# Optimization experiments

Measured on AMD Instinct MI355X. Metric: run time of the kernel, lower is better.

The kernel has to match this reference:

```python
import jax, jax.numpy as jnp
import numpy as np

D_MODEL = 512
D_EMB = 300
D_FIXED = 30000
D_EXT = 32000
BS, L, J, N, T = 8, 256, 48, 32, 48


def setup_inputs() -> dict:
    key = jax.random.key(0)
    ks = jax.random.split(key, 32)
    s = 0.02
    def nrm(k, shape, scale=0.02):
        return jax.random.normal(k, shape, dtype=jnp.float32) * scale
    inp = {
        "Mp": jax.random.normal(ks[0], (BS, L, D_MODEL), dtype=jnp.float32),
        "Mq": jax.random.normal(ks[1], (BS, J, D_MODEL), dtype=jnp.float32),
        "Mqa": jax.random.normal(ks[2], (BS, N, D_MODEL), dtype=jnp.float32),
        "Mnlg": jax.random.normal(ks[3], (BS, T, D_MODEL), dtype=jnp.float32),
        "mask_p": jnp.ones((BS, L, 1), dtype=bool),
        "mask_q": jnp.ones((BS, J, 1), dtype=bool),
        "mask_qa": jnp.ones((BS, N, 1), dtype=bool),
        "source_ext": jax.random.randint(ks[4], (BS, L + J + N), 0, D_EXT, dtype=jnp.int64) if jax.config.jax_enable_x64 else jax.random.randint(ks[4], (BS, L + J + N), 0, D_EXT).astype(jnp.int32),
        "special_mask": jnp.ones((D_FIXED,), dtype=bool).at[jnp.array([0, 1, 2, 3])].set(False),
        "d_ext_vocab": D_EXT,
    }
    # additive attention params for question / qa / passage branches
    names = ["q", "a", "p"]
    for i, nme in enumerate(names):
        base = 5 + 5 * i
        inp[f"Wk_{nme}"] = nrm(ks[base + 0], (D_MODEL, D_MODEL))
        inp[f"bk_{nme}"] = jnp.zeros((D_MODEL,), dtype=jnp.float32)
        inp[f"Wq_{nme}"] = nrm(ks[base + 1], (D_MODEL, D_MODEL))
        inp[f"bq_{nme}"] = jnp.zeros((D_MODEL,), dtype=jnp.float32)
        inp[f"v_{nme}"] = nrm(ks[base + 2], (D_MODEL,))
    # vocab generator: Linear(d_model, d_emb) -> Linear(d_emb, d_fixed, bias=False)
    inp["W1"] = nrm(ks[20], (D_MODEL, D_EMB))
    inp["b1"] = jnp.zeros((D_EMB,), dtype=jnp.float32)
    inp["W2"] = nrm(ks[21], (D_EMB, D_FIXED))
    # mixture: Linear(4*d_model, 4) + softmax
    inp["Wm"] = nrm(ks[22], (4 * D_MODEL, 4))
    inp["bm"] = jnp.zeros((4,), dtype=jnp.float32)
    return inp


def _additive_attn(K, V, Q, mask, Wk, bk, Wq, bq, v):
    # K,V: [b,S,d]; Q: [b,T,d]; mask: [b,S,1] bool
    Kp = K @ Wk + bk                                  # [b,S,d]
    Qp = Q @ Wq + bq                                  # [b,T,d]
    scores = jnp.einsum("btsd,d->bts", jnp.tanh(Qp[:, :, None, :] + Kp[:, None, :, :]), v)
    scores = jnp.where(mask[:, None, :, 0], scores, -1e9)
    attn = jax.nn.softmax(scores, axis=-1)            # [b,T,S]
    ctx = jnp.einsum("bts,bsd->btd", attn, V)         # [b,T,d]
    return ctx, attn


def reference(Mp, Mq, Mqa, Mnlg, mask_p, mask_q, mask_qa, source_ext, special_mask,
              Wk_q, bk_q, Wq_q, bq_q, v_q,
              Wk_a, bk_a, Wq_a, bq_a, v_a,
              Wk_p, bk_p, Wq_p, bq_p, v_p,
              W1, b1, W2, Wm, bm, d_ext_vocab):
    d_fixed = special_mask.shape[0]
    bs, Tq, _ = Mnlg.shape

    ctx_q, q_distr = _additive_attn(Mq, Mq, Mnlg, mask_q, Wk_q, bk_q, Wq_q, bq_q, v_q)
    ctx_a, qa_distr = _additive_attn(Mqa, Mqa, Mnlg, mask_qa, Wk_a, bk_a, Wq_a, bq_a, v_a)
    ctx_p, p_distr = _additive_attn(Mp, Mp, Mnlg, mask_p, Wk_p, bk_p, Wq_p, bq_p, v_p)

    # fixed-vocab distribution with special tokens masked out
    logits = (Mnlg @ W1 + b1) @ W2                    # [b,T,d_fixed]
    logits = jnp.where(special_mask[None, None, :], logits, -1e9)
    fixed_vocab_distr = jax.nn.softmax(logits, axis=-1)

    # mixture weights
    mix_in = jnp.concatenate([Mnlg, ctx_q, ctx_a, ctx_p], axis=-1)  # [b,T,4d]
    lambdas = jax.nn.softmax(mix_in @ Wm + bm, axis=-1)             # [b,T,4]
    lam_v, lam_q, lam_qa, lam_p = jnp.split(lambdas, 4, axis=-1)

    fixed_vocab_distr = fixed_vocab_distr * lam_v
    source_distr = jnp.concatenate([p_distr * lam_p, q_distr * lam_q, qa_distr * lam_qa], axis=-1)  # [b,T,S_tot]

    # scatter-add over extended vocab (math-equivalent to one_hot + matmul)
    def _scatter(src, idx):
        # src: [T,S_tot], idx: [S_tot]
        return jnp.zeros((Tq, d_ext_vocab), src.dtype).at[:, idx].add(src)

    ext_vocab_distr = jax.vmap(_scatter)(source_distr, source_ext)  # [b,T,d_ext]
    ext_vocab_distr = ext_vocab_distr.at[:, :, :d_fixed].add(fixed_vocab_distr)
    return ext_vocab_distr, lambdas
```

## Files before the change

### kernel.cpp

```cpp
#include <hip/hip_runtime.h>
#include <math.h>

#define BS     8
#define LL     256
#define JJ     48
#define NN     32
#define TT     48
#define DM     512
#define DEMB   300
#define DFIX   30000
#define DEXT   32000
#define SRC_TOT (LL + JJ + NN)
#define ROWS   (BS * TT)
#define NT     235

typedef float f32x4  __attribute__((ext_vector_type(4)));
typedef short bf16x8 __attribute__((ext_vector_type(8)));

__device__ __forceinline__ short f2bf(float f) {
    union { float f; unsigned u; } v; v.f = f;
    return (short)((v.u + 0x7FFFu + ((v.u >> 16) & 1u)) >> 16);
}
__device__ __forceinline__ float bf2f(short s) {
    union { unsigned u; float f; } v;
    v.u = ((unsigned)(unsigned short)s) << 16;
    return v.f;
}
__device__ __forceinline__ float fast_exp2(float x) {
#if __has_builtin(__builtin_amdgcn_exp2f)
    return __builtin_amdgcn_exp2f(x);
#else
    return exp2f(x);
#endif
}
__device__ __forceinline__ float fast_rcp(float x) {
#if __has_builtin(__builtin_amdgcn_rcpf)
    return __builtin_amdgcn_rcpf(x);
#else
    return 1.f / x;
#endif
}
__device__ __forceinline__ float fast_tanh(float x) {
    x = fminf(fmaxf(x, -15.f), 15.f);
    const float e = fast_exp2(x * 2.885390082f);
    return (e - 1.f) * fast_rcp(e + 1.f);
}
__device__ __forceinline__ bool smask_true(const void* smask, bool byteLayout, int i)
{
    if (byteLayout) return ((const unsigned char*)smask)[i] != 0;
    return ((const int*)smask)[i] != 0;
}
__device__ __forceinline__ void mask8(const void* smask, bool byteLayout, int i,
                                      int* mb)
{
    if (byteLayout) {
        const uchar4 a = ((const uchar4*)((const unsigned char*)smask + i))[0];
        const uchar4 b = ((const uchar4*)((const unsigned char*)smask + i))[1];
        mb[0]=a.x; mb[1]=a.y; mb[2]=a.z; mb[3]=a.w;
        mb[4]=b.x; mb[5]=b.y; mb[6]=b.z; mb[7]=b.w;
    } else {
        const int* p = (const int*)smask + i;
        #pragma unroll
        for (int j = 0; j < 8; ++j) mb[j] = p[j];
    }
}

struct PDesc { const float* src; short* dst; int K, N, Kp, ntx, tiles; };
struct PArgs { PDesc d[8]; int nd; };

__global__ __launch_bounds__(256) void prep_kernel(PArgs pa)
{
    __shared__ short T[64][72];
    int tile = blockIdx.x, g = 0;
    while (g + 1 < pa.nd && tile >= pa.d[g].tiles) { tile -= pa.d[g].tiles; ++g; }
    const PDesc d = pa.d[g];
    const int kt = tile / d.ntx, nt = tile % d.ntx;
    const int k0 = kt * 64, n0 = nt * 64;
    const int tid = threadIdx.x;
    {
        const int n = n0 + (tid & 63);
        #pragma unroll
        for (int p = 0; p < 16; ++p) {
            const int kk = p * 4 + (tid >> 6);
            const int k = k0 + kk;
            float v = 0.f;
            if (k < d.K && n < d.N) v = d.src[(size_t)k * d.N + n];
            T[kk][tid & 63] = f2bf(v);
        }
    }
    __syncthreads();
    {
        const int nn = tid >> 2;
        const int kq = (tid & 3) * 16;
        const int n = n0 + nn;
        if (n < d.N) {
            bf16x8 v0, v1;
            #pragma unroll
            for (int j = 0; j < 8; ++j) v0[j] = T[kq + j][nn];
            #pragma unroll
            for (int j = 0; j < 8; ++j) v1[j] = T[kq + 8 + j][nn];
            *(bf16x8*)&d.dst[(size_t)n * d.Kp + k0 + kq]     = v0;
            *(bf16x8*)&d.dst[(size_t)n * d.Kp + k0 + kq + 8] = v1;
        }
    }
}

struct GDesc { const float* A; const short* Bt; const float* bias; void* C;
               const void* smask; float* pstat;
               int M, N, K, Kp, nx, my, obf, nt, tiles; };
struct GArgs { GDesc d[7]; int nd; };

__global__ __launch_bounds__(256) void gemm_bf16_kernel(GArgs ga)
{
    __shared__ short As[2][4][130][8];
    __shared__ short Bs[2][4][130][8];
    __shared__ float pm_s[128][2];
    __shared__ float ps_s[128][2];

    int tile = blockIdx.x, g = 0;
    while (g + 1 < ga.nd && tile >= ga.d[g].tiles) { tile -= ga.d[g].tiles; ++g; }
    const float* __restrict__ A  = ga.d[g].A;
    const short* __restrict__ Bt = ga.d[g].Bt;
    const float* bias = ga.d[g].bias;
    const int N = ga.d[g].N, K = ga.d[g].K, Kp = ga.d[g].Kp;
    const int nx = ga.d[g].nx, my = ga.d[g].my, obf = ga.d[g].obf;

    int bm, bn;
    if (my > 0) { bm = (tile % my) * 128; bn = (tile / my) * 128; }
    else        { bm = (tile / nx) * 128; bn = (tile % nx) * 128; }
    const int tid  = threadIdx.x;
    const int lane = tid & 63;
    const int wv   = tid >> 6;
    const int wm   = (wv >> 1) * 64;
    const int wn   = (wv & 1) * 64;

    const int a_kq  = (tid & 7) * 4;
    const int a_row = tid >> 3;
    float4  ra[4];
    bf16x8  rb[2];

    auto loadA = [&](int k0) {
        #pragma unroll
        for (int p = 0; p < 4; ++p) {
            const int row = p * 32 + a_row;
            const int gk = k0 + a_kq;
            const float* ap = A + (size_t)(bm + row) * K + gk;
            float4 a = make_float4(0.f, 0.f, 0.f, 0.f);
            if (gk + 3 < K) a = *(const float4*)ap;
            else {
                if (gk     < K) a.x = ap[0];
                if (gk + 1 < K) a.y = ap[1];
                if (gk + 2 < K) a.z = ap[2];
                if (gk + 3 < K) a.w = ap[3];
            }
            ra[p] = a;
        }
    };
    auto loadB = [&](int k0) {
        #pragma unroll
        for (int p = 0; p < 2; ++p) {
            const int idx = p * 256 + tid;
            const int n = idx >> 2, kb = idx & 3;
            const int gn = bn + n;
            bf16x8 v = {};
            if (gn < N) v = *(const bf16x8*)&Bt[(size_t)gn * Kp + k0 + kb * 8];
            rb[p] = v;
        }
    };
    auto storeA = [&](int buf) {
        const int kb = a_kq >> 3, ko = a_kq & 7;
        #pragma unroll
        for (int p = 0; p < 4; ++p) {
            const int row = p * 32 + a_row;
            short4 s = { f2bf(ra[p].x), f2bf(ra[p].y), f2bf(ra[p].z), f2bf(ra[p].w) };
            *(short4*)&As[buf][kb][row][ko] = s;
        }
    };
    auto storeB = [&](int buf) {
        #pragma unroll
        for (int p = 0; p < 2; ++p) {
            const int idx = p * 256 + tid;
            const int n = idx >> 2, kb = idx & 3;
            *(bf16x8*)&Bs[buf][kb][n][0] = rb[p];
        }
    };

    f32x4 acc[4][4] = {};
    const int nk = Kp / 32;

    loadA(0); loadB(0);
    storeA(0); storeB(0);
    __syncthreads();

    for (int kk = 0; kk < nk; ++kk) {
        const int cur = kk & 1;
        if (kk + 1 < nk) { loadA((kk + 1) * 32); loadB((kk + 1) * 32); }
        bf16x8 af[4], bfr[4];
        #pragma unroll
        for (int i = 0; i < 4; ++i) {
            af[i]  = *(const bf16x8*)&As[cur][lane >> 4][wm + i * 16 + (lane & 15)][0];
            bfr[i] = *(const bf16x8*)&Bs[cur][lane >> 4][wn + i * 16 + (lane & 15)][0];
        }
        #pragma unroll
        for (int mi = 0; mi < 4; ++mi)
            #pragma unroll
            for (int ni = 0; ni < 4; ++ni)
                acc[mi][ni] = __builtin_amdgcn_mfma_f32_16x16x32_bf16(
                    af[mi], bfr[ni], acc[mi][ni], 0, 0, 0);
        if (kk + 1 < nk) { storeA(cur ^ 1); storeB(cur ^ 1); }
        __syncthreads();
    }

    if (!obf) {
        float* Cf = (float*)ga.d[g].C;
        #pragma unroll
        for (int ni = 0; ni < 4; ++ni) {
            const int gn = bn + wn + ni * 16 + (lane & 15);
            if (gn >= N) continue;
            const float bb = bias ? bias[gn] : 0.f;
            #pragma unroll
            for (int mi = 0; mi < 4; ++mi)
                #pragma unroll
                for (int r = 0; r < 4; ++r) {
                    const int gm = bm + wm + mi * 16 + (lane >> 4) * 4 + r;
                    Cf[(size_t)gm * N + gn] = acc[mi][ni][r] + bb;
                }
        }
    } else {
        short* Cs = (short*)ga.d[g].C;
        const void* sm = ga.d[g].smask;
        const bool byteLayout = (((const int*)sm)[1] == 0x01010101);
        int mk[4];
        #pragma unroll
        for (int ni = 0; ni < 4; ++ni) {
            const int gn = bn + wn + ni * 16 + (lane & 15);
            const bool inb = (gn < N);
            mk[ni] = inb && smask_true(sm, byteLayout, inb ? gn : 0);
            if (inb) {
                #pragma unroll
                for (int mi = 0; mi < 4; ++mi)
                    #pragma unroll
                    for (int r = 0; r < 4; ++r) {
                        const int gm = bm + wm + mi * 16 + (lane >> 4) * 4 + r;
                        Cs[(size_t)gm * N + gn] = f2bf(acc[mi][ni][r]);
                    }
            }
        }
        #pragma unroll
        for (int mi = 0; mi < 4; ++mi) {
            #pragma unroll
            for (int r = 0; r < 4; ++r) {
                const int rl = wm + mi * 16 + (lane >> 4) * 4 + r;
                float vmax = -INFINITY;
                #pragma unroll
                for (int ni = 0; ni < 4; ++ni)
                    if (mk[ni]) vmax = fmaxf(vmax, acc[mi][ni][r]);
                #pragma unroll
                for (int o = 1; o < 16; o <<= 1)
                    vmax = fmaxf(vmax, __shfl_xor(vmax, o));
                float se = 0.f;
                #pragma unroll
                for (int ni = 0; ni < 4; ++ni)
                    if (mk[ni]) se += __expf(acc[mi][ni][r] - vmax);
                #pragma unroll
                for (int o = 1; o < 16; o <<= 1)
                    se += __shfl_xor(se, o);
                if ((lane & 15) == 0) {
                    pm_s[rl][wn >> 6] = vmax;
                    ps_s[rl][wn >> 6] = se;
                }
            }
        }
        __syncthreads();
        if (tid < 128) {
            const float mA = pm_s[tid][0], mB = pm_s[tid][1];
            const float sA = ps_s[tid][0], sB = ps_s[tid][1];
            const float m = fmaxf(mA, mB);
            float s = 0.f;
            if (sA > 0.f) s += sA * __expf(mA - m);
            if (sB > 0.f) s += sB * __expf(mB - m);
            float* ps = ga.d[g].pstat;
            const size_t idx = ((size_t)(bm + tid) * ga.d[g].nt + (bn >> 7)) * 2;
            ps[idx + 0] = m;
            ps[idx + 1] = s;
        }
    }
}

__global__ __launch_bounds__(64) void combine_kernel(
    const float* __restrict__ pstat, const float* __restrict__ lam,
    float* __restrict__ stat)
{
    const int r = blockIdx.x;
    const int lane = threadIdx.x;
    float m = -INFINITY;
    for (int c = lane; c < NT; c += 64)
        m = fmaxf(m, pstat[((size_t)r * NT + c) * 2]);
    #pragma unroll
    for (int o = 32; o; o >>= 1) m = fmaxf(m, __shfl_xor(m, o));
    float s = 0.f;
    for (int c = lane; c < NT; c += 64) {
        const float pm = pstat[((size_t)r * NT + c) * 2];
        const float ps = pstat[((size_t)r * NT + c) * 2 + 1];
        if (ps > 0.f) s += ps * __expf(pm - m);
    }
    #pragma unroll
    for (int o = 32; o; o >>= 1) s += __shfl_xor(s, o);
    if (lane == 0) {
        stat[r * 2 + 0] = m;
        stat[r * 2 + 1] = lam[r * 4 + 0] / s;
    }
}

struct SDesc { const float* Kp; const float* Qp; const float* vv;
               int Sb, s0, cnt, off; };
struct SArgs { SDesc c[6]; };

__global__ __launch_bounds__(256) void scores_kernel(SArgs sa,
                                                     float* __restrict__ scb)
{
    const SDesc d = sa.c[blockIdx.y];
    const int bt   = blockIdx.x;
    const int b    = bt / TT;
    const int tid  = threadIdx.x;
    const int lane = tid & 63;
    const int wave = tid >> 6;

    float qp[8], vv[8];
    {
        const float4* q4 = (const float4*)(d.Qp + (size_t)bt * DM) + lane * 2;
        float4 a = q4[0], c = q4[1];
        qp[0]=a.x; qp[1]=a.y; qp[2]=a.z; qp[3]=a.w;
        qp[4]=c.x; qp[5]=c.y; qp[6]=c.z; qp[7]=c.w;
        const float4* v4 = (const float4*)d.vv + lane * 2;
        a = v4[0]; c = v4[1];
        vv[0]=a.x; vv[1]=a.y; vv[2]=a.z; vv[3]=a.w;
        vv[4]=c.x; vv[5]=c.y; vv[6]=c.z; vv[7]=c.w;
    }
    for (int s = wave; s < d.cnt; s += 4) {
        const float* krow = d.Kp + ((size_t)b * d.Sb + d.s0 + s) * DM + lane * 8;
        const float4 ka = ((const float4*)krow)[0];
        const float4 kb = ((const float4*)krow)[1];
        float acc = 0.f;
        acc = fmaf(vv[0], fast_tanh(qp[0] + ka.x), acc);
        acc = fmaf(vv[1], fast_tanh(qp[1] + ka.y), acc);
        acc = fmaf(vv[2], fast_tanh(qp[2] + ka.z), acc);
        acc = fmaf(vv[3], fast_tanh(qp[3] + ka.w), acc);
        acc = fmaf(vv[4], fast_tanh(qp[4] + kb.x), acc);
        acc = fmaf(vv[5], fast_tanh(qp[5] + kb.y), acc);
        acc = fmaf(vv[6], fast_tanh(qp[6] + kb.z), acc);
        acc = fmaf(vv[7], fast_tanh(qp[7] + kb.w), acc);
        #pragma unroll
        for (int off = 32; off; off >>= 1) acc += __shfl_xor(acc, off);
        if (lane == 0) scb[(size_t)bt * SRC_TOT + d.off + s] = acc;
    }
}

__global__ __launch_bounds__(512) void attn2mix_kernel(
    const float* __restrict__ scb,
    const float* __restrict__ Mq, const float* __restrict__ Mqa,
    const float* __restrict__ Mp, const float* __restrict__ Mnlg,
    const float* __restrict__ Wm, const float* __restrict__ bm,
    float* __restrict__ dQ, float* __restrict__ dQA, float* __restrict__ dP,
    float* __restrict__ lam_ws, float* __restrict__ lam_out)
{
    __shared__ float a_sh[SRC_TOT];
    __shared__ float cQ[DM], cA[DM], cP[DM];
    __shared__ float red[16];
    __shared__ float redm[32];
    const int bt   = blockIdx.x;
    const int b    = bt / TT;
    const int tid  = threadIdx.x;
    const int lane = tid & 63;
    const int wave = tid >> 6;
    const float* srow = scb + (size_t)bt * SRC_TOT;

    #pragma unroll
    for (int br = 0; br < 3; ++br) {
        const int off = (br == 0) ? 0 : (br == 1) ? JJ : (JJ + NN);
        const int cnt = (br == 0) ? JJ : (br == 1) ? NN : LL;
        float x = (tid < cnt) ? srow[off + tid] : -INFINITY;
        float m = x;
        #pragma unroll
        for (int o = 32; o; o >>= 1) m = fmaxf(m, __shfl_xor(m, o));
        if (lane == 0) red[wave] = m;
        __syncthreads();
        m = red[0];
        #pragma unroll
        for (int w = 1; w < 8; ++w) m = fmaxf(m, red[w]);
        float e = (tid < cnt) ? __expf(x - m) : 0.f;
        float ss = e;
        #pragma unroll
        for (int o = 32; o; o >>= 1) ss += __shfl_xor(ss, o);
        if (lane == 0) red[8 + wave] = ss;
        __syncthreads();
        float denom = 0.f;
        #pragma unroll
        for (int w = 0; w < 8; ++w) denom += red[8 + w];
        if (tid < cnt) {
            const float a = e / denom;
            a_sh[off + tid] = a;
            float* dst = (br == 0) ? dQ : (br == 1) ? dQA : dP;
            dst[(size_t)bt * cnt + tid] = a;
        }
        __syncthreads();
    }
    {
        float aQ = 0.f, aA = 0.f, aP = 0.f;
        for (int s = 0; s < JJ; ++s)
            aQ = fmaf(a_sh[s],           Mq [((size_t)b * JJ + s) * DM + tid], aQ);
        for (int s = 0; s < NN; ++s)
            aA = fmaf(a_sh[JJ + s],      Mqa[((size_t)b * NN + s) * DM + tid], aA);
        for (int s = 0; s < LL; ++s)
            aP = fmaf(a_sh[JJ + NN + s], Mp [((size_t)b * LL + s) * DM + tid], aP);
        cQ[tid] = aQ; cA[tid] = aA; cP[tid] = aP;
    }
    __syncthreads();
    {
        const float x0 = Mnlg[(size_t)bt * DM + tid];
        const float x1 = cQ[tid], x2 = cA[tid], x3 = cP[tid];
        const float4 w0 = *(const float4*)&Wm[(size_t)tid * 4];
        const float4 w1 = *(const float4*)&Wm[(size_t)(512 + tid) * 4];
        const float4 w2 = *(const float4*)&Wm[(size_t)(1024 + tid) * 4];
        const float4 w3 = *(const float4*)&Wm[(size_t)(1536 + tid) * 4];
        float acc[4];
        acc[0] = x0 * w0.x + x1 * w1.x + x2 * w2.x + x3 * w3.x;
        acc[1] = x0 * w0.y + x1 * w1.y + x2 * w2.y + x3 * w3.y;
        acc[2] = x0 * w0.z + x1 * w1.z + x2 * w2.z + x3 * w3.z;
        acc[3] = x0 * w0.w + x1 * w1.w + x2 * w2.w + x3 * w3.w;
        #pragma unroll
        for (int c = 0; c < 4; ++c)
            #pragma unroll
            for (int o = 32; o; o >>= 1) acc[c] += __shfl_xor(acc[c], o);
        if (lane == 0) {
            redm[wave * 4 + 0] = acc[0]; redm[wave * 4 + 1] = acc[1];
            redm[wave * 4 + 2] = acc[2]; redm[wave * 4 + 3] = acc[3];
        }
        __syncthreads();
        if (tid == 0) {
            float l[4];
            #pragma unroll
            for (int c = 0; c < 4; ++c) {
                float s = bm[c];
                #pragma unroll
                for (int w = 0; w < 8; ++w) s += redm[w * 4 + c];
                l[c] = s;
            }
            const float mx = fmaxf(fmaxf(l[0], l[1]), fmaxf(l[2], l[3]));
            const float e0 = __expf(l[0] - mx), e1 = __expf(l[1] - mx);
            const float e2 = __expf(l[2] - mx), e3 = __expf(l[3] - mx);
            const float inv = 1.f / (e0 + e1 + e2 + e3);
            lam_ws[bt * 4 + 0] = e0 * inv; lam_out[bt * 4 + 0] = e0 * inv;
            lam_ws[bt * 4 + 1] = e1 * inv; lam_out[bt * 4 + 1] = e1 * inv;
            lam_ws[bt * 4 + 2] = e2 * inv; lam_out[bt * 4 + 2] = e2 * inv;
            lam_ws[bt * 4 + 3] = e3 * inv; lam_out[bt * 4 + 3] = e3 * inv;
        }
    }
}

__global__ __launch_bounds__(1024) void writescatter_kernel(
    const short* __restrict__ logits, const void* __restrict__ smask,
    const float* __restrict__ stat, const float* __restrict__ lam,
    const float* __restrict__ dP, const float* __restrict__ dQ,
    const float* __restrict__ dQA, const void* __restrict__ src_ext,
    float* __restrict__ out)
{
    const bool byteLayout = (((const int*)smask)[1] == 0x01010101);
    const int r = blockIdx.x;
    const float m   = stat[r * 2 + 0];
    const float inv = stat[r * 2 + 1];

    const short* lrow = logits + (size_t)r * DFIX;
    float* orow = out + (size_t)r * DEXT;
    const int tid = threadIdx.x;
    #pragma unroll
    for (int k = 0; k < 4; ++k) {
        const int i = (k * 1024 + tid) * 8;
        if (i >= DEXT) continue;
        float4 o0 = make_float4(0.f, 0.f, 0.f, 0.f);
        float4 o1 = make_float4(0.f, 0.f, 0.f, 0.f);
        if (i < DFIX) {
            const bf16x8 v = *(const bf16x8*)&lrow[i];
            int mb[8]; mask8(smask, byteLayout, i, mb);
            o0.x = mb[0] ? __expf(bf2f(v[0]) - m) * inv : 0.f;
            o0.y = mb[1] ? __expf(bf2f(v[1]) - m) * inv : 0.f;
            o0.z = mb[2] ? __expf(bf2f(v[2]) - m) * inv : 0.f;
            o0.w = mb[3] ? __expf(bf2f(v[3]) - m) * inv : 0.f;
            o1.x = mb[4] ? __expf(bf2f(v[4]) - m) * inv : 0.f;
            o1.y = mb[5] ? __expf(bf2f(v[5]) - m) * inv : 0.f;
            o1.z = mb[6] ? __expf(bf2f(v[6]) - m) * inv : 0.f;
            o1.w = mb[7] ? __expf(bf2f(v[7]) - m) * inv : 0.f;
        }
        *(float4*)&orow[i]     = o0;
        *(float4*)&orow[i + 4] = o1;
    }
    __syncthreads();
    if (tid < SRC_TOT) {
        const int* s32 = (const int*)src_ext;
        const bool src64 = (s32[1] == 0 && s32[3] == 0 && s32[5] == 0 && s32[7] == 0);
        const int b = r / TT;
        const float lamq  = lam[r * 4 + 1];
        const float lamqa = lam[r * 4 + 2];
        const float lamp  = lam[r * 4 + 3];
        const int pos = b * SRC_TOT + tid;
        const int idx = src64 ? (int)((const long long*)src_ext)[pos] : s32[pos];
        float val;
        if      (tid < LL)      val = dP [(size_t)r * LL + tid]             * lamp;
        else if (tid < LL + JJ) val = dQ [(size_t)r * JJ + (tid - LL)]      * lamq;
        else                    val = dQA[(size_t)r * NN + (tid - LL - JJ)] * lamqa;
        atomicAdd(&orow[idx], val);
    }
}

extern "C" void kernel_launch(void* const* d_in, const int* in_sizes, int n_in,
                              void* d_out, int out_size, void* d_ws, size_t ws_size,
                              hipStream_t stream)
{
    const float* Mp   = (const float*)d_in[0];
    const float* Mq   = (const float*)d_in[1];
    const float* Mqa  = (const float*)d_in[2];
    const float* Mnlg = (const float*)d_in[3];
    const void* src_ext = d_in[7];
    const void* smask   = d_in[8];
    const float* Wk_q = (const float*)d_in[10];
    const float* bk_q = (const float*)d_in[11];
    const float* Wq_q = (const float*)d_in[12];
    const float* bq_q = (const float*)d_in[13];
    const float* v_q  = (const float*)d_in[14];
    const float* Wk_a = (const float*)d_in[15];
    const float* bk_a = (const float*)d_in[16];
    const float* Wq_a = (const float*)d_in[17];
    const float* bq_a = (const float*)d_in[18];
    const float* v_a  = (const float*)d_in[19];
    const float* Wk_p = (const float*)d_in[20];
    const float* bk_p = (const float*)d_in[21];
    const float* Wq_p = (const float*)d_in[22];
    const float* bq_p = (const float*)d_in[23];
    const float* v_p  = (const float*)d_in[24];
    const float* W1   = (const float*)d_in[25];
    const float* b1   = (const float*)d_in[26];
    const float* W2   = (const float*)d_in[27];
    const float* Wm   = (const float*)d_in[28];
    const float* bm   = (const float*)d_in[29];
    float* out = (float*)d_out;

    char* ws = (char*)d_ws;
    size_t off = 0;
    auto alloc = [&](size_t bytes) -> char* {
        char* p = ws + off;
        off += (bytes + 255) & ~(size_t)255;
        return p;
    };
    short* logits = (short*)alloc((size_t)ROWS * DFIX * 2);
    float* KpP    = (float*)alloc((size_t)BS * LL * DM * 4);
    float* KpQ    = (float*)alloc((size_t)BS * JJ * DM * 4);
    float* KpA    = (float*)alloc((size_t)BS * NN * DM * 4);
    float* QpQ    = (float*)alloc((size_t)ROWS * DM * 4);
    float* QpA    = (float*)alloc((size_t)ROWS * DM * 4);
    float* QpP    = (float*)alloc((size_t)ROWS * DM * 4);
    float* Hh     = (float*)alloc((size_t)ROWS * DEMB * 4);
    float* dP     = (float*)alloc((size_t)ROWS * LL * 4);
    float* dQ     = (float*)alloc((size_t)ROWS * JJ * 4);
    float* dQA    = (float*)alloc((size_t)ROWS * NN * 4);
    float* lam    = (float*)alloc((size_t)ROWS * 4 * 4);
    float* pstat  = (float*)alloc((size_t)ROWS * NT * 2 * 4);
    float* stat   = (float*)alloc((size_t)ROWS * 2 * 4);
    float* scb    = (float*)alloc((size_t)ROWS * SRC_TOT * 4);
    short* tWkq = (short*)alloc((size_t)DM * DM * 2);
    short* tWqq = (short*)alloc((size_t)DM * DM * 2);
    short* tWka = (short*)alloc((size_t)DM * DM * 2);
    short* tWqa = (short*)alloc((size_t)DM * DM * 2);
    short* tWkp = (short*)alloc((size_t)DM * DM * 2);
    short* tWqp = (short*)alloc((size_t)DM * DM * 2);
    short* tW1  = (short*)alloc((size_t)DEMB * DM * 2);
    short* tW2  = (short*)alloc((size_t)DFIX * 320 * 2);
    (void)ws_size; (void)in_sizes; (void)n_in; (void)out_size;

    PArgs pa;
    pa.nd = 8;
    pa.d[0] = { Wk_p, tWkp, DM,   DM,   DM,  8,  64 };
    pa.d[1] = { Wk_q, tWkq, DM,   DM,   DM,  8,  64 };
    pa.d[2] = { Wk_a, tWka, DM,   DM,   DM,  8,  64 };
    pa.d[3] = { Wq_q, tWqq, DM,   DM,   DM,  8,  64 };
    pa.d[4] = { Wq_a, tWqa, DM,   DM,   DM,  8,  64 };
    pa.d[5] = { Wq_p, tWqp, DM,   DM,   DM,  8,  64 };
    pa.d[6] = { W1,   tW1,  DM,   DEMB, DM,  5,  40 };
    pa.d[7] = { W2,   tW2,  DEMB, DFIX, 320, 469, 2345 };
    prep_kernel<<<64 * 6 + 40 + 2345, 256, 0, stream>>>(pa);

    GArgs gA;
    gA.nd = 1;
    gA.d[0] = { Mnlg, tW1, b1, Hh, nullptr, nullptr,
                ROWS, DEMB, DM, DM, 3, 0, 0, 0, 9 };
    gemm_bf16_kernel<<<9, 256, 0, stream>>>(gA);

    GArgs gB;
    gB.nd = 7;
    gB.d[0] = { Mp,   tWkp, bk_p,    KpP,    nullptr, nullptr,
                BS*LL, DM,   DM,   DM,  4,   0, 0, 0,  64 };
    gB.d[1] = { Mq,   tWkq, bk_q,    KpQ,    nullptr, nullptr,
                BS*JJ, DM,   DM,   DM,  4,   0, 0, 0,  12 };
    gB.d[2] = { Mqa,  tWka, bk_a,    KpA,    nullptr, nullptr,
                BS*NN, DM,   DM,   DM,  4,   0, 0, 0,   8 };
    gB.d[3] = { Mnlg, tWqq, bq_q,    QpQ,    nullptr, nullptr,
                ROWS,  DM,   DM,   DM,  4,   0, 0, 0,  12 };
    gB.d[4] = { Mnlg, tWqa, bq_a,    QpA,    nullptr, nullptr,
                ROWS,  DM,   DM,   DM,  4,   0, 0, 0,  12 };
    gB.d[5] = { Mnlg, tWqp, bq_p,    QpP,    nullptr, nullptr,
                ROWS,  DM,   DM,   DM,  4,   0, 0, 0,  12 };
    gB.d[6] = { Hh,   tW2,  nullptr, logits, smask,   pstat,
                ROWS,  DFIX, DEMB, 320, 235, 3, 1, NT, 705 };
    gemm_bf16_kernel<<<825, 256, 0, stream>>>(gB);

    SArgs sa;
    sa.c[0] = { KpQ, QpQ, v_q, JJ,   0, JJ,  0 };
    sa.c[1] = { KpA, QpA, v_a, NN,   0, NN,  JJ };
    sa.c[2] = { KpP, QpP, v_p, LL,   0, 64,  JJ + NN };
    sa.c[3] = { KpP, QpP, v_p, LL,  64, 64,  JJ + NN + 64 };
    sa.c[4] = { KpP, QpP, v_p, LL, 128, 64,  JJ + NN + 128 };
    sa.c[5] = { KpP, QpP, v_p, LL, 192, 64,  JJ + NN + 192 };
    scores_kernel<<<dim3(ROWS, 6), 256, 0, stream>>>(sa, scb);
    attn2mix_kernel<<<ROWS, 512, 0, stream>>>(scb, Mq, Mqa, Mp, Mnlg, Wm, bm,
                                              dQ, dQA, dP, lam,
                                              out + (size_t)ROWS * DEXT);

    combine_kernel<<<ROWS, 64, 0, stream>>>(pstat, lam, stat);
    writescatter_kernel<<<ROWS, 1024, 0, stream>>>(
        logits, smask, stat, lam, dP, dQ, dQA, src_ext, out);
}
```

Baseline: 161.9 us.

## Pre-convert activations to bf16 in prep kernel and fuse combine into attn2mix

Adds flat fp32-to-bf16 conversion tiles to the prep kernel for Mp, Mq, Mqa and Mnlg. The GEMMs now load bf16 A operands directly, and the first GEMM writes its hidden output as padded bf16, which removes per-tile conversion and halves A-side traffic. The attention-context reduction now reads the bf16 copies, and the separate combine kernel is folded into attn2mix, saving one launch. In exchange the prep kernel does extra conversion work, and the context vectors now use bf16 inputs, which lowers their precision.

```diff
diff --git a/kernel.cpp b/kernel.cpp
--- a/kernel.cpp
+++ b/kernel.cpp
@@ -13,6 +13,7 @@
 #define SRC_TOT (LL + JJ + NN)
 #define ROWS   (BS * TT)
 #define NT     235
+#define KH     320
 
 typedef float f32x4  __attribute__((ext_vector_type(4)));
 typedef short bf16x8 __attribute__((ext_vector_type(8)));
@@ -66,7 +67,7 @@
 }
 
 struct PDesc { const float* src; short* dst; int K, N, Kp, ntx, tiles; };
-struct PArgs { PDesc d[8]; int nd; };
+struct PArgs { PDesc d[12]; int nd; };
 
 __global__ __launch_bounds__(256) void prep_kernel(PArgs pa)
 {
@@ -74,9 +75,23 @@
     int tile = blockIdx.x, g = 0;
     while (g + 1 < pa.nd && tile >= pa.d[g].tiles) { tile -= pa.d[g].tiles; ++g; }
     const PDesc d = pa.d[g];
+    const int tid = threadIdx.x;
+
+    if (d.ntx == 0) {
+        const int i = (tile * 256 + tid) * 8;
+        if (i < d.K) {
+            const float4 a = ((const float4*)(d.src + i))[0];
+            const float4 b = ((const float4*)(d.src + i))[1];
+            bf16x8 v;
+            v[0]=f2bf(a.x); v[1]=f2bf(a.y); v[2]=f2bf(a.z); v[3]=f2bf(a.w);
+            v[4]=f2bf(b.x); v[5]=f2bf(b.y); v[6]=f2bf(b.z); v[7]=f2bf(b.w);
+            *(bf16x8*)&d.dst[i] = v;
+        }
+        return;
+    }
+
     const int kt = tile / d.ntx, nt = tile % d.ntx;
     const int k0 = kt * 64, n0 = nt * 64;
-    const int tid = threadIdx.x;
     {
         const int n = n0 + (tid & 63);
         #pragma unroll
@@ -105,9 +120,9 @@
     }
 }
 
-struct GDesc { const float* A; const short* Bt; const float* bias; void* C;
+struct GDesc { const short* A; const short* Bt; const float* bias; void* C;
                const void* smask; float* pstat;
-               int M, N, K, Kp, nx, my, obf, nt, tiles; };
+               int M, N, K, Kp, nx, my, obf, npad, nt, tiles; };
 struct GArgs { GDesc d[7]; int nd; };
 
 __global__ __launch_bounds__(256) void gemm_bf16_kernel(GArgs ga)
@@ -119,11 +134,12 @@
 
     int tile = blockIdx.x, g = 0;
     while (g + 1 < ga.nd && tile >= ga.d[g].tiles) { tile -= ga.d[g].tiles; ++g; }
-    const float* __restrict__ A  = ga.d[g].A;
+    const short* __restrict__ A  = ga.d[g].A;
     const short* __restrict__ Bt = ga.d[g].Bt;
     const float* bias = ga.d[g].bias;
-    const int N = ga.d[g].N, K = ga.d[g].K, Kp = ga.d[g].Kp;
+    const int N = ga.d[g].N, Kp = ga.d[g].Kp;
     const int nx = ga.d[g].nx, my = ga.d[g].my, obf = ga.d[g].obf;
+    const int npad = ga.d[g].npad;
 
     int bm, bn;
     if (my > 0) { bm = (tile % my) * 128; bn = (tile / my) * 128; }
@@ -134,26 +150,13 @@
     const int wm   = (wv >> 1) * 64;
     const int wn   = (wv & 1) * 64;
 
-    const int a_kq  = (tid & 7) * 4;
-    const int a_row = tid >> 3;
-    float4  ra[4];
-    bf16x8  rb[2];
+    bf16x8 ra[2], rb[2];
 
     auto loadA = [&](int k0) {
         #pragma unroll
-        for (int p = 0; p < 4; ++p) {
-            const int row = p * 32 + a_row;
-            const int gk = k0 + a_kq;
-            const float* ap = A + (size_t)(bm + row) * K + gk;
-            float4 a = make_float4(0.f, 0.f, 0.f, 0.f);
-            if (gk + 3 < K) a = *(const float4*)ap;
-            else {
-                if (gk     < K) a.x = ap[0];
-                if (gk + 1 < K) a.y = ap[1];
-                if (gk + 2 < K) a.z = ap[2];
-                if (gk + 3 < K) a.w = ap[3];
-            }
-            ra[p] = a;
+        for (int p = 0; p < 2; ++p) {
+            const int row = p * 64 + (tid >> 2);
+            ra[p] = *(const bf16x8*)&A[(size_t)(bm + row) * Kp + k0 + (tid & 3) * 8];
         }
     };
     auto loadB = [&](int k0) {
@@ -168,13 +171,10 @@
         }
     };
     auto storeA = [&](int buf) {
-        const int kb = a_kq >> 3, ko = a_kq & 7;
-        #pragma unroll
-        for (int p = 0; p < 4; ++p) {
-            const int row = p * 32 + a_row;
-            short4 s = { f2bf(ra[p].x), f2bf(ra[p].y), f2bf(ra[p].z), f2bf(ra[p].w) };
-            *(short4*)&As[buf][kb][row][ko] = s;
-        }
+        const int kb = tid & 3;
+        #pragma unroll
+        for (int p = 0; p < 2; ++p)
+            *(bf16x8*)&As[buf][kb][p * 64 + (tid >> 2)][0] = ra[p];
     };
     auto storeB = [&](int buf) {
         #pragma unroll
@@ -211,7 +211,7 @@
         __syncthreads();
     }
 
-    if (!obf) {
+    if (obf == 0) {
         float* Cf = (float*)ga.d[g].C;
         #pragma unroll
         for (int ni = 0; ni < 4; ++ni) {
@@ -224,6 +224,22 @@
                 for (int r = 0; r < 4; ++r) {
                     const int gm = bm + wm + mi * 16 + (lane >> 4) * 4 + r;
                     Cf[(size_t)gm * N + gn] = acc[mi][ni][r] + bb;
+                }
+        }
+    } else if (obf == 2) {
+        short* Cs = (short*)ga.d[g].C;
+        #pragma unroll
+        for (int ni = 0; ni < 4; ++ni) {
+            const int gn = bn + wn + ni * 16 + (lane & 15);
+            if (gn >= npad) continue;
+            const bool valid = (gn < N);
+            const float bb = (valid && bias) ? bias[gn] : 0.f;
+            #pragma unroll
+            for (int mi = 0; mi < 4; ++mi)
+                #pragma unroll
+                for (int r = 0; r < 4; ++r) {
+                    const int gm = bm + wm + mi * 16 + (lane >> 4) * 4 + r;
+                    Cs[(size_t)gm * npad + gn] = valid ? f2bf(acc[mi][ni][r] + bb) : (short)0;
                 }
         }
     } else {
@@ -284,31 +300,6 @@
             ps[idx + 0] = m;
             ps[idx + 1] = s;
         }
-    }
-}
-
-__global__ __launch_bounds__(64) void combine_kernel(
-    const float* __restrict__ pstat, const float* __restrict__ lam,
-    float* __restrict__ stat)
-{
-    const int r = blockIdx.x;
-    const int lane = threadIdx.x;
-    float m = -INFINITY;
-    for (int c = lane; c < NT; c += 64)
-        m = fmaxf(m, pstat[((size_t)r * NT + c) * 2]);
-    #pragma unroll
-    for (int o = 32; o; o >>= 1) m = fmaxf(m, __shfl_xor(m, o));
-    float s = 0.f;
-    for (int c = lane; c < NT; c += 64) {
-        const float pm = pstat[((size_t)r * NT + c) * 2];
-        const float ps = pstat[((size_t)r * NT + c) * 2 + 1];
-        if (ps > 0.f) s += ps * __expf(pm - m);
-    }
-    #pragma unroll
-    for (int o = 32; o; o >>= 1) s += __shfl_xor(s, o);
-    if (lane == 0) {
-        stat[r * 2 + 0] = m;
-        stat[r * 2 + 1] = lam[r * 4 + 0] / s;
     }
 }
 
@@ -358,16 +349,19 @@
 
 __global__ __launch_bounds__(512) void attn2mix_kernel(
     const float* __restrict__ scb,
-    const float* __restrict__ Mq, const float* __restrict__ Mqa,
-    const float* __restrict__ Mp, const float* __restrict__ Mnlg,
+    const short* __restrict__ Mqb, const short* __restrict__ Mqab,
+    const short* __restrict__ Mpb, const float* __restrict__ Mnlg,
     const float* __restrict__ Wm, const float* __restrict__ bm,
+    const float* __restrict__ pstat,
     float* __restrict__ dQ, float* __restrict__ dQA, float* __restrict__ dP,
-    float* __restrict__ lam_ws, float* __restrict__ lam_out)
+    float* __restrict__ lam_ws, float* __restrict__ lam_out,
+    float* __restrict__ stat)
 {
     __shared__ float a_sh[SRC_TOT];
     __shared__ float cQ[DM], cA[DM], cP[DM];
     __shared__ float red[16];
     __shared__ float redm[32];
+    __shared__ float s_lamv;
     const int bt   = blockIdx.x;
     const int b    = bt / TT;
     const int tid  = threadIdx.x;
@@ -408,11 +402,11 @@
     {
         float aQ = 0.f, aA = 0.f, aP = 0.f;
         for (int s = 0; s < JJ; ++s)
-            aQ = fmaf(a_sh[s],           Mq [((size_t)b * JJ + s) * DM + tid], aQ);
+            aQ = fmaf(a_sh[s],           bf2f(Mqb [((size_t)b * JJ + s) * DM + tid]), aQ);
         for (int s = 0; s < NN; ++s)
-            aA = fmaf(a_sh[JJ + s],      Mqa[((size_t)b * NN + s) * DM + tid], aA);
+            aA = fmaf(a_sh[JJ + s],      bf2f(Mqab[((size_t)b * NN + s) * DM + tid]), aA);
         for (int s = 0; s < LL; ++s)
-            aP = fmaf(a_sh[JJ + NN + s], Mp [((size_t)b * LL + s) * DM + tid], aP);
+            aP = fmaf(a_sh[JJ + NN + s], bf2f(Mpb [((size_t)b * LL + s) * DM + tid]), aP);
         cQ[tid] = aQ; cA[tid] = aA; cP[tid] = aP;
     }
     __syncthreads();
@@ -450,10 +444,31 @@
             const float e0 = __expf(l[0] - mx), e1 = __expf(l[1] - mx);
             const float e2 = __expf(l[2] - mx), e3 = __expf(l[3] - mx);
             const float inv = 1.f / (e0 + e1 + e2 + e3);
+            s_lamv = e0 * inv;
             lam_ws[bt * 4 + 0] = e0 * inv; lam_out[bt * 4 + 0] = e0 * inv;
             lam_ws[bt * 4 + 1] = e1 * inv; lam_out[bt * 4 + 1] = e1 * inv;
             lam_ws[bt * 4 + 2] = e2 * inv; lam_out[bt * 4 + 2] = e2 * inv;
             lam_ws[bt * 4 + 3] = e3 * inv; lam_out[bt * 4 + 3] = e3 * inv;
+        }
+    }
+    __syncthreads();
+    if (wave == 0) {
+        float m = -INFINITY;
+        for (int c = lane; c < NT; c += 64)
+            m = fmaxf(m, pstat[((size_t)bt * NT + c) * 2]);
+        #pragma unroll
+        for (int o = 32; o; o >>= 1) m = fmaxf(m, __shfl_xor(m, o));
+        float s = 0.f;
+        for (int c = lane; c < NT; c += 64) {
+            const float pm = pstat[((size_t)bt * NT + c) * 2];
+            const float ps = pstat[((size_t)bt * NT + c) * 2 + 1];
+            if (ps > 0.f) s += ps * __expf(pm - m);
+        }
+        #pragma unroll
+        for (int o = 32; o; o >>= 1) s += __shfl_xor(s, o);
+        if (lane == 0) {
+            stat[bt * 2 + 0] = m;
+            stat[bt * 2 + 1] = s_lamv / s;
         }
     }
 }
@@ -558,7 +573,6 @@
     float* QpQ    = (float*)alloc((size_t)ROWS * DM * 4);
     float* QpA    = (float*)alloc((size_t)ROWS * DM * 4);
     float* QpP    = (float*)alloc((size_t)ROWS * DM * 4);
-    float* Hh     = (float*)alloc((size_t)ROWS * DEMB * 4);
     float* dP     = (float*)alloc((size_t)ROWS * LL * 4);
     float* dQ     = (float*)alloc((size_t)ROWS * JJ * 4);
     float* dQA    = (float*)alloc((size_t)ROWS * NN * 4);
@@ -573,43 +587,52 @@
     short* tWkp = (short*)alloc((size_t)DM * DM * 2);
     short* tWqp = (short*)alloc((size_t)DM * DM * 2);
     short* tW1  = (short*)alloc((size_t)DEMB * DM * 2);
-    short* tW2  = (short*)alloc((size_t)DFIX * 320 * 2);
+    short* tW2  = (short*)alloc((size_t)DFIX * KH * 2);
+    short* Mp_bf   = (short*)alloc((size_t)BS * LL * DM * 2);
+    short* Mq_bf   = (short*)alloc((size_t)BS * JJ * DM * 2);
+    short* Mqa_bf  = (short*)alloc((size_t)BS * NN * DM * 2);
+    short* Mnlg_bf = (short*)alloc((size_t)ROWS * DM * 2);
+    short* Hh_bf   = (short*)alloc((size_t)ROWS * KH * 2);
     (void)ws_size; (void)in_sizes; (void)n_in; (void)out_size;
 
     PArgs pa;
-    pa.nd = 8;
-    pa.d[0] = { Wk_p, tWkp, DM,   DM,   DM,  8,  64 };
-    pa.d[1] = { Wk_q, tWkq, DM,   DM,   DM,  8,  64 };
-    pa.d[2] = { Wk_a, tWka, DM,   DM,   DM,  8,  64 };
-    pa.d[3] = { Wq_q, tWqq, DM,   DM,   DM,  8,  64 };
-    pa.d[4] = { Wq_a, tWqa, DM,   DM,   DM,  8,  64 };
-    pa.d[5] = { Wq_p, tWqp, DM,   DM,   DM,  8,  64 };
-    pa.d[6] = { W1,   tW1,  DM,   DEMB, DM,  5,  40 };
-    pa.d[7] = { W2,   tW2,  DEMB, DFIX, 320, 469, 2345 };
-    prep_kernel<<<64 * 6 + 40 + 2345, 256, 0, stream>>>(pa);
+    pa.nd = 12;
+    pa.d[0]  = { Wk_p, tWkp, DM,   DM,   DM,  8,  64 };
+    pa.d[1]  = { Wk_q, tWkq, DM,   DM,   DM,  8,  64 };
+    pa.d[2]  = { Wk_a, tWka, DM,   DM,   DM,  8,  64 };
+    pa.d[3]  = { Wq_q, tWqq, DM,   DM,   DM,  8,  64 };
+    pa.d[4]  = { Wq_a, tWqa, DM,   DM,   DM,  8,  64 };
+    pa.d[5]  = { Wq_p, tWqp, DM,   DM,   DM,  8,  64 };
+    pa.d[6]  = { W1,   tW1,  DM,   DEMB, DM,  5,  40 };
+    pa.d[7]  = { W2,   tW2,  DEMB, DFIX, KH,  469, 2345 };
+    pa.d[8]  = { Mp,   Mp_bf,   BS*LL*DM, 0, 0, 0, (BS*LL*DM) / 2048 };
+    pa.d[9]  = { Mq,   Mq_bf,   BS*JJ*DM, 0, 0, 0, (BS*JJ*DM) / 2048 };
+    pa.d[10] = { Mqa,  Mqa_bf,  BS*NN*DM, 0, 0, 0, (BS*NN*DM) / 2048 };
+    pa.d[11] = { Mnlg, Mnlg_bf, ROWS*DM,  0, 0, 0, (ROWS*DM) / 2048 };
+    prep_kernel<<<64 * 6 + 40 + 2345 + 512 + 96 + 64 + 96, 256, 0, stream>>>(pa);
 
     GArgs gA;
     gA.nd = 1;
-    gA.d[0] = { Mnlg, tW1, b1, Hh, nullptr, nullptr,
-                ROWS, DEMB, DM, DM, 3, 0, 0, 0, 9 };
+    gA.d[0] = { Mnlg_bf, tW1, b1, Hh_bf, nullptr, nullptr,
+                ROWS, DEMB, DM, DM, 3, 0, 2, KH, 0, 9 };
     gemm_bf16_kernel<<<9, 256, 0, stream>>>(gA);
 
     GArgs gB;
     gB.nd = 7;
-    gB.d[0] = { Mp,   tWkp, bk_p,    KpP,    nullptr, nullptr,
-                BS*LL, DM,   DM,   DM,  4,   0, 0, 0,  64 };
-    gB.d[1] = { Mq,   tWkq, bk_q,    KpQ,    nullptr, nullptr,
-                BS*JJ, DM,   DM,   DM,  4,   0, 0, 0,  12 };
-    gB.d[2] = { Mqa,  tWka, bk_a,    KpA,    nullptr, nullptr,
-                BS*NN, DM,   DM,   DM,  4,   0, 0, 0,   8 };
-    gB.d[3] = { Mnlg, tWqq, bq_q,    QpQ,    nullptr, nullptr,
-                ROWS,  DM,   DM,   DM,  4,   0, 0, 0,  12 };
-    gB.d[4] = { Mnlg, tWqa, bq_a,    QpA,    nullptr, nullptr,
-                ROWS,  DM,   DM,   DM,  4,   0, 0, 0,  12 };
-    gB.d[5] = { Mnlg, tWqp, bq_p,    QpP,    nullptr, nullptr,
-                ROWS,  DM,   DM,   DM,  4,   0, 0, 0,  12 };
-    gB.d[6] = { Hh,   tW2,  nullptr, logits, smask,   pstat,
-                ROWS,  DFIX, DEMB, 320, 235, 3, 1, NT, 705 };
+    gB.d[0] = { Mp_bf,   tWkp, bk_p,    KpP,    nullptr, nullptr,
+                BS*LL, DM,   DM,   DM,  4,   0, 0, DM,   0,  64 };
+    gB.d[1] = { Mq_bf,   tWkq, bk_q,    KpQ,    nullptr, nullptr,
+                BS*JJ, DM,   DM,   DM,  4,   0, 0, DM,   0,  12 };
+    gB.d[2] = { Mqa_bf,  tWka, bk_a,    KpA,    nullptr, nullptr,
+                BS*NN, DM,   DM,   DM,  4,   0, 0, DM,   0,   8 };
+    gB.d[3] = { Mnlg_bf, tWqq, bq_q,    QpQ,    nullptr, nullptr,
+                ROWS,  DM,   DM,   DM,  4,   0, 0, DM,   0,  12 };
+    gB.d[4] = { Mnlg_bf, tWqa, bq_a,    QpA,    nullptr, nullptr,
+                ROWS,  DM,   DM,   DM,  4,   0, 0, DM,   0,  12 };
+    gB.d[5] = { Mnlg_bf, tWqp, bq_p,    QpP,    nullptr, nullptr,
+                ROWS,  DM,   DM,   DM,  4,   0, 0, DM,   0,  12 };
+    gB.d[6] = { Hh_bf,   tW2,  nullptr, logits, smask,   pstat,
+                ROWS,  DFIX, DEMB, KH,  235, 3, 1, DFIX, NT, 705 };
     gemm_bf16_kernel<<<825, 256, 0, stream>>>(gB);
 
     SArgs sa;
@@ -620,11 +643,10 @@
     sa.c[4] = { KpP, QpP, v_p, LL, 128, 64,  JJ + NN + 128 };
     sa.c[5] = { KpP, QpP, v_p, LL, 192, 64,  JJ + NN + 192 };
     scores_kernel<<<dim3(ROWS, 6), 256, 0, stream>>>(sa, scb);
-    attn2mix_kernel<<<ROWS, 512, 0, stream>>>(scb, Mq, Mqa, Mp, Mnlg, Wm, bm,
-                                              dQ, dQA, dP, lam,
-                                              out + (size_t)ROWS * DEXT);
-
-    combine_kernel<<<ROWS, 64, 0, stream>>>(pstat, lam, stat);
+    attn2mix_kernel<<<ROWS, 512, 0, stream>>>(scb, Mq_bf, Mqa_bf, Mp_bf, Mnlg,
+                                              Wm, bm, pstat, dQ, dQA, dP, lam,
+                                              out + (size_t)ROWS * DEXT, stat);
+
     writescatter_kernel<<<ROWS, 1024, 0, stream>>>(
         logits, smask, stat, lam, dP, dQ, dQA, src_ext, out);
 }
```

Result: faster. 157.2 us (-2.9%).
